# Optimization experiments

Measured on AMD Instinct MI355X. Metric: run time of the kernel, lower is better.

The kernel has to match this reference:

```python
import jax, jax.numpy as jnp
import numpy as np

B = 8192
MAX_ATOMS = 768
EPS = 1e-7


def setup_inputs() -> dict:
    key = jax.random.key(0)
    k1, k2, k3 = jax.random.split(key, 3)
    inp = jax.random.normal(k1, (B, 3 * MAX_ATOMS), dtype=jnp.float32)
    tgt = jax.random.normal(k2, (B, 3 * MAX_ATOMS), dtype=jnp.float32)
    # variable atom counts; keep >= MAX_ATOMS//2 so centering/division is well-posed
    num_atoms = jax.random.randint(k3, (B,), MAX_ATOMS // 2, MAX_ATOMS + 1, dtype=jnp.int64)
    return {"input": inp, "target": tgt, "num_atoms": num_atoms}


def _kabsch_rmsd(inp, tgt, num_atoms):
    b = inp.shape[0]
    m = inp.shape[1] // 3
    X = inp.reshape(b, m, 3)
    Y = tgt.reshape(b, m, 3)
    mask = (jnp.arange(m)[None, :] < num_atoms[:, None])[..., None]  # [B, M, 1]
    n = num_atoms.astype(inp.dtype)[:, None]  # [B, 1]
    # center over the valid atoms of each sample
    Xc = (X - (jnp.where(mask, X, 0).sum(axis=1) / n)[:, None, :])
    Yc = (Y - (jnp.where(mask, Y, 0).sum(axis=1) / n)[:, None, :])
    Xc = jnp.where(mask, Xc, 0)
    Yc = jnp.where(mask, Yc, 0)
    # 3x3 correlation matrix per sample (Kabsch)
    R = jnp.einsum('bai,baj->bij', Xc, Yc)  # [B, 3, 3]
    s = jnp.linalg.svd(R, compute_uv=False)  # [B, 3], descending
    d = jnp.sign(jnp.linalg.det(R))  # proper-rotation correction
    trace = s[:, 0] + s[:, 1] + d * s[:, 2]
    e = jnp.sum(Xc * Xc, axis=(1, 2)) + jnp.sum(Yc * Yc, axis=(1, 2)) - 2.0 * trace
    n1 = num_atoms.astype(inp.dtype)
    return jnp.sqrt(jnp.maximum(e, 0.0) / n1 + EPS)


def reference(input, target, num_atoms):
    return _kabsch_rmsd(input, target, num_atoms)
```

## Files before the change

kernel.cpp:

```cpp
#include <hip/hip_runtime.h>
#include <math.h>

#ifndef M_PI
#define M_PI 3.14159265358979323846
#endif

#define MA 768

__device__ __forceinline__ float wred64(float v) {
#pragma unroll
    for (int off = 32; off; off >>= 1) v += __shfl_xor(v, off, 64);
    return v;
}

__global__ __launch_bounds__(256) void kabsch_rmsd_kernel(
    const float* __restrict__ inp, const float* __restrict__ tgt,
    const int* __restrict__ natoms, float* __restrict__ out)
{
    const int wave = threadIdx.x >> 6;
    const int lane = threadIdx.x & 63;
    const int b = blockIdx.x * 4 + wave;
    const int n = natoms[b];
    const float* __restrict__ X = inp + (size_t)b * (3 * MA);
    const float* __restrict__ Y = tgt + (size_t)b * (3 * MA);

    float sx0 = 0.f, sx1 = 0.f, sx2 = 0.f;
    float sy0 = 0.f, sy1 = 0.f, sy2 = 0.f;
    float c00 = 0.f, c01 = 0.f, c02 = 0.f;
    float c10 = 0.f, c11 = 0.f, c12 = 0.f;
    float c20 = 0.f, c21 = 0.f, c22 = 0.f;
    float nx2 = 0.f, ny2 = 0.f;

    auto acc = [&](float x0, float x1, float x2, float y0, float y1, float y2) {
        sx0 += x0; sx1 += x1; sx2 += x2;
        sy0 += y0; sy1 += y1; sy2 += y2;
        c00 = fmaf(x0, y0, c00); c01 = fmaf(x0, y1, c01); c02 = fmaf(x0, y2, c02);
        c10 = fmaf(x1, y0, c10); c11 = fmaf(x1, y1, c11); c12 = fmaf(x1, y2, c12);
        c20 = fmaf(x2, y0, c20); c21 = fmaf(x2, y1, c21); c22 = fmaf(x2, y2, c22);
        nx2 = fmaf(x0, x0, nx2); nx2 = fmaf(x1, x1, nx2); nx2 = fmaf(x2, x2, nx2);
        ny2 = fmaf(y0, y0, ny2); ny2 = fmaf(y1, y1, ny2); ny2 = fmaf(y2, y2, ny2);
    };

#pragma unroll
    for (int it = 0; it < 3; ++it) {
        const int base = it * 256 + lane * 4;
        if (base < n) {
            const float4* px = (const float4*)(X + 3 * base);
            const float4* py = (const float4*)(Y + 3 * base);
            float4 fx0 = px[0], fx1 = px[1], fx2 = px[2];
            float4 fy0 = py[0], fy1 = py[1], fy2 = py[2];

            acc(fx0.x, fx0.y, fx0.z, fy0.x, fy0.y, fy0.z);
            {
                bool v = (base + 1) < n;
                float x0 = v ? fx0.w : 0.f, x1 = v ? fx1.x : 0.f, x2 = v ? fx1.y : 0.f;
                float y0 = v ? fy0.w : 0.f, y1 = v ? fy1.x : 0.f, y2 = v ? fy1.y : 0.f;
                acc(x0, x1, x2, y0, y1, y2);
            }
            {
                bool v = (base + 2) < n;
                float x0 = v ? fx1.z : 0.f, x1 = v ? fx1.w : 0.f, x2 = v ? fx2.x : 0.f;
                float y0 = v ? fy1.z : 0.f, y1 = v ? fy1.w : 0.f, y2 = v ? fy2.x : 0.f;
                acc(x0, x1, x2, y0, y1, y2);
            }
            {
                bool v = (base + 3) < n;
                float x0 = v ? fx2.y : 0.f, x1 = v ? fx2.z : 0.f, x2 = v ? fx2.w : 0.f;
                float y0 = v ? fy2.y : 0.f, y1 = v ? fy2.z : 0.f, y2 = v ? fy2.w : 0.f;
                acc(x0, x1, x2, y0, y1, y2);
            }
        }
    }

    sx0 = wred64(sx0); sx1 = wred64(sx1); sx2 = wred64(sx2);
    sy0 = wred64(sy0); sy1 = wred64(sy1); sy2 = wred64(sy2);
    c00 = wred64(c00); c01 = wred64(c01); c02 = wred64(c02);
    c10 = wred64(c10); c11 = wred64(c11); c12 = wred64(c12);
    c20 = wred64(c20); c21 = wred64(c21); c22 = wred64(c22);
    nx2 = wred64(nx2); ny2 = wred64(ny2);

    if (lane == 0) {
        const double dn = (double)n;

        double R00 = (double)c00 - (double)sx0 * (double)sy0 / dn;
        double R01 = (double)c01 - (double)sx0 * (double)sy1 / dn;
        double R02 = (double)c02 - (double)sx0 * (double)sy2 / dn;
        double R10 = (double)c10 - (double)sx1 * (double)sy0 / dn;
        double R11 = (double)c11 - (double)sx1 * (double)sy1 / dn;
        double R12 = (double)c12 - (double)sx1 * (double)sy2 / dn;
        double R20 = (double)c20 - (double)sx2 * (double)sy0 / dn;
        double R21 = (double)c21 - (double)sx2 * (double)sy1 / dn;
        double R22 = (double)c22 - (double)sx2 * (double)sy2 / dn;
        double ex = (double)nx2 -
            ((double)sx0 * sx0 + (double)sx1 * sx1 + (double)sx2 * sx2) / dn;
        double ey = (double)ny2 -
            ((double)sy0 * sy0 + (double)sy1 * sy1 + (double)sy2 * sy2) / dn;

        double A00 = R00 * R00 + R10 * R10 + R20 * R20;
        double A11 = R01 * R01 + R11 * R11 + R21 * R21;
        double A22 = R02 * R02 + R12 * R12 + R22 * R22;
        double A01 = R00 * R01 + R10 * R11 + R20 * R21;
        double A02 = R00 * R02 + R10 * R12 + R20 * R22;
        double A12 = R01 * R02 + R11 * R12 + R21 * R22;

        double detR = R00 * (R11 * R22 - R12 * R21)
                    - R01 * (R10 * R22 - R12 * R20)
                    + R02 * (R10 * R21 - R11 * R20);

        double q = (A00 + A11 + A22) / 3.0;
        double p1 = A01 * A01 + A02 * A02 + A12 * A12;
        double b00 = A00 - q, b11 = A11 - q, b22 = A22 - q;
        double p2 = b00 * b00 + b11 * b11 + b22 * b22 + 2.0 * p1;
        double e0, e1, e2;
        if (p2 <= 0.0) {
            e0 = e1 = e2 = q;
        } else {
            double p = sqrt(p2 / 6.0);
            double ip = 1.0 / p;
            double B00 = b00 * ip, B11 = b11 * ip, B22 = b22 * ip;
            double B01 = A01 * ip, B02 = A02 * ip, B12 = A12 * ip;
            double detB = B00 * (B11 * B22 - B12 * B12)
                        - B01 * (B01 * B22 - B12 * B02)
                        + B02 * (B01 * B12 - B11 * B02);
            double r = 0.5 * detB;
            r = fmin(1.0, fmax(-1.0, r));
            double phi = acos(r) / 3.0;
            e0 = q + 2.0 * p * cos(phi);
            e2 = q + 2.0 * p * cos(phi + 2.0 * M_PI / 3.0);
            e1 = 3.0 * q - e0 - e2;
        }
        double s0 = sqrt(fmax(e0, 0.0));
        double s1 = sqrt(fmax(e1, 0.0));
        double s2 = sqrt(fmax(e2, 0.0));
        double d = (detR > 0.0) ? 1.0 : ((detR < 0.0) ? -1.0 : 0.0);
        double tr = s0 + s1 + d * s2;
        double e = ex + ey - 2.0 * tr;
        out[b] = (float)sqrt(fmax(e, 0.0) / dn + 1e-7);
    }
}

extern "C" void kernel_launch(void* const* d_in, const int* in_sizes, int n_in,
                              void* d_out, int out_size, void* d_ws, size_t ws_size,
                              hipStream_t stream) {
    const float* inp = (const float*)d_in[0];
    const float* tgt = (const float*)d_in[1];
    const int* natoms = (const int*)d_in[2];
    float* out = (float*)d_out;
    (void)d_ws; (void)ws_size; (void)n_in; (void)in_sizes;
    kabsch_rmsd_kernel<<<dim3(out_size / 4), dim3(256), 0, stream>>>(inp, tgt, natoms, out);
}
```

Before: 29.72 us.

## Split Kabsch into reduction and per-thread eigen finish kernels with DPP reductions

The single kernel is split in two. The first reduces per-sample sums using DPP row operations instead of shuffle-xor and writes 17 partial sums per sample to workspace in SoA layout. The second kernel runs the double-precision 3x3 eigen and SVD finish with one thread per sample, so the serial lane-0 tail no longer stalls each wave. In exchange it adds a second launch and a workspace round-trip, and it hardcodes NB=8192.

```diff
diff --git a/kernel.cpp b/kernel.cpp
--- a/kernel.cpp
+++ b/kernel.cpp
@@ -6,16 +6,21 @@
 #endif
 
 #define MA 768
+#define NB 8192
 
-__device__ __forceinline__ float wred64(float v) {
-#pragma unroll
-    for (int off = 32; off; off >>= 1) v += __shfl_xor(v, off, 64);
+__device__ __forceinline__ float dpp_red_add(float v) {
+    v += __int_as_float(__builtin_amdgcn_update_dpp(0, __float_as_int(v), 0x111, 0xf, 0xf, true));
+    v += __int_as_float(__builtin_amdgcn_update_dpp(0, __float_as_int(v), 0x112, 0xf, 0xf, true));
+    v += __int_as_float(__builtin_amdgcn_update_dpp(0, __float_as_int(v), 0x114, 0xf, 0xe, true));
+    v += __int_as_float(__builtin_amdgcn_update_dpp(0, __float_as_int(v), 0x118, 0xf, 0xc, true));
+    v += __int_as_float(__builtin_amdgcn_update_dpp(0, __float_as_int(v), 0x142, 0xa, 0xf, true));
+    v += __int_as_float(__builtin_amdgcn_update_dpp(0, __float_as_int(v), 0x143, 0xc, 0xf, true));
     return v;
 }
 
-__global__ __launch_bounds__(256) void kabsch_rmsd_kernel(
+__global__ __launch_bounds__(256) void kabsch_reduce_kernel(
     const float* __restrict__ inp, const float* __restrict__ tgt,
-    const int* __restrict__ natoms, float* __restrict__ out)
+    const int* __restrict__ natoms, float* __restrict__ ws)
 {
     const int wave = threadIdx.x >> 6;
     const int lane = threadIdx.x & 63;
@@ -53,90 +58,108 @@
             acc(fx0.x, fx0.y, fx0.z, fy0.x, fy0.y, fy0.z);
             {
                 bool v = (base + 1) < n;
-                float x0 = v ? fx0.w : 0.f, x1 = v ? fx1.x : 0.f, x2 = v ? fx1.y : 0.f;
-                float y0 = v ? fy0.w : 0.f, y1 = v ? fy1.x : 0.f, y2 = v ? fy1.y : 0.f;
-                acc(x0, x1, x2, y0, y1, y2);
+                acc(v ? fx0.w : 0.f, v ? fx1.x : 0.f, v ? fx1.y : 0.f,
+                    v ? fy0.w : 0.f, v ? fy1.x : 0.f, v ? fy1.y : 0.f);
             }
             {
                 bool v = (base + 2) < n;
-                float x0 = v ? fx1.z : 0.f, x1 = v ? fx1.w : 0.f, x2 = v ? fx2.x : 0.f;
-                float y0 = v ? fy1.z : 0.f, y1 = v ? fy1.w : 0.f, y2 = v ? fy2.x : 0.f;
-                acc(x0, x1, x2, y0, y1, y2);
+                acc(v ? fx1.z : 0.f, v ? fx1.w : 0.f, v ? fx2.x : 0.f,
+                    v ? fy1.z : 0.f, v ? fy1.w : 0.f, v ? fy2.x : 0.f);
             }
             {
                 bool v = (base + 3) < n;
-                float x0 = v ? fx2.y : 0.f, x1 = v ? fx2.z : 0.f, x2 = v ? fx2.w : 0.f;
-                float y0 = v ? fy2.y : 0.f, y1 = v ? fy2.z : 0.f, y2 = v ? fy2.w : 0.f;
-                acc(x0, x1, x2, y0, y1, y2);
+                acc(v ? fx2.y : 0.f, v ? fx2.z : 0.f, v ? fx2.w : 0.f,
+                    v ? fy2.y : 0.f, v ? fy2.z : 0.f, v ? fy2.w : 0.f);
             }
         }
     }
 
-    sx0 = wred64(sx0); sx1 = wred64(sx1); sx2 = wred64(sx2);
-    sy0 = wred64(sy0); sy1 = wred64(sy1); sy2 = wred64(sy2);
-    c00 = wred64(c00); c01 = wred64(c01); c02 = wred64(c02);
-    c10 = wred64(c10); c11 = wred64(c11); c12 = wred64(c12);
-    c20 = wred64(c20); c21 = wred64(c21); c22 = wred64(c22);
-    nx2 = wred64(nx2); ny2 = wred64(ny2);
+    sx0 = dpp_red_add(sx0); sx1 = dpp_red_add(sx1); sx2 = dpp_red_add(sx2);
+    sy0 = dpp_red_add(sy0); sy1 = dpp_red_add(sy1); sy2 = dpp_red_add(sy2);
+    c00 = dpp_red_add(c00); c01 = dpp_red_add(c01); c02 = dpp_red_add(c02);
+    c10 = dpp_red_add(c10); c11 = dpp_red_add(c11); c12 = dpp_red_add(c12);
+    c20 = dpp_red_add(c20); c21 = dpp_red_add(c21); c22 = dpp_red_add(c22);
+    nx2 = dpp_red_add(nx2); ny2 = dpp_red_add(ny2);
 
-    if (lane == 0) {
-        const double dn = (double)n;
+    if (lane == 63) {
+        ws[ 0 * NB + b] = sx0; ws[ 1 * NB + b] = sx1; ws[ 2 * NB + b] = sx2;
+        ws[ 3 * NB + b] = sy0; ws[ 4 * NB + b] = sy1; ws[ 5 * NB + b] = sy2;
+        ws[ 6 * NB + b] = c00; ws[ 7 * NB + b] = c01; ws[ 8 * NB + b] = c02;
+        ws[ 9 * NB + b] = c10; ws[10 * NB + b] = c11; ws[11 * NB + b] = c12;
+        ws[12 * NB + b] = c20; ws[13 * NB + b] = c21; ws[14 * NB + b] = c22;
+        ws[15 * NB + b] = nx2; ws[16 * NB + b] = ny2;
+    }
+}
 
-        double R00 = (double)c00 - (double)sx0 * (double)sy0 / dn;
-        double R01 = (double)c01 - (double)sx0 * (double)sy1 / dn;
-        double R02 = (double)c02 - (double)sx0 * (double)sy2 / dn;
-        double R10 = (double)c10 - (double)sx1 * (double)sy0 / dn;
-        double R11 = (double)c11 - (double)sx1 * (double)sy1 / dn;
-        double R12 = (double)c12 - (double)sx1 * (double)sy2 / dn;
-        double R20 = (double)c20 - (double)sx2 * (double)sy0 / dn;
-        double R21 = (double)c21 - (double)sx2 * (double)sy1 / dn;
-        double R22 = (double)c22 - (double)sx2 * (double)sy2 / dn;
-        double ex = (double)nx2 -
-            ((double)sx0 * sx0 + (double)sx1 * sx1 + (double)sx2 * sx2) / dn;
-        double ey = (double)ny2 -
-            ((double)sy0 * sy0 + (double)sy1 * sy1 + (double)sy2 * sy2) / dn;
+__global__ __launch_bounds__(256) void kabsch_finish_kernel(
+    const float* __restrict__ ws, const int* __restrict__ natoms,
+    float* __restrict__ out)
+{
+    const int b = blockIdx.x * 256 + threadIdx.x;
+    const int n = natoms[b];
+    const double dn = (double)n;
 
-        double A00 = R00 * R00 + R10 * R10 + R20 * R20;
-        double A11 = R01 * R01 + R11 * R11 + R21 * R21;
-        double A22 = R02 * R02 + R12 * R12 + R22 * R22;
-        double A01 = R00 * R01 + R10 * R11 + R20 * R21;
-        double A02 = R00 * R02 + R10 * R12 + R20 * R22;
-        double A12 = R01 * R02 + R11 * R12 + R21 * R22;
+    const float sx0 = ws[ 0 * NB + b], sx1 = ws[ 1 * NB + b], sx2 = ws[ 2 * NB + b];
+    const float sy0 = ws[ 3 * NB + b], sy1 = ws[ 4 * NB + b], sy2 = ws[ 5 * NB + b];
+    const float c00 = ws[ 6 * NB + b], c01 = ws[ 7 * NB + b], c02 = ws[ 8 * NB + b];
+    const float c10 = ws[ 9 * NB + b], c11 = ws[10 * NB + b], c12 = ws[11 * NB + b];
+    const float c20 = ws[12 * NB + b], c21 = ws[13 * NB + b], c22 = ws[14 * NB + b];
+    const float nx2 = ws[15 * NB + b], ny2 = ws[16 * NB + b];
 
-        double detR = R00 * (R11 * R22 - R12 * R21)
-                    - R01 * (R10 * R22 - R12 * R20)
-                    + R02 * (R10 * R21 - R11 * R20);
+    double R00 = (double)c00 - (double)sx0 * (double)sy0 / dn;
+    double R01 = (double)c01 - (double)sx0 * (double)sy1 / dn;
+    double R02 = (double)c02 - (double)sx0 * (double)sy2 / dn;
+    double R10 = (double)c10 - (double)sx1 * (double)sy0 / dn;
+    double R11 = (double)c11 - (double)sx1 * (double)sy1 / dn;
+    double R12 = (double)c12 - (double)sx1 * (double)sy2 / dn;
+    double R20 = (double)c20 - (double)sx2 * (double)sy0 / dn;
+    double R21 = (double)c21 - (double)sx2 * (double)sy1 / dn;
+    double R22 = (double)c22 - (double)sx2 * (double)sy2 / dn;
+    double ex = (double)nx2 -
+        ((double)sx0 * sx0 + (double)sx1 * sx1 + (double)sx2 * sx2) / dn;
+    double ey = (double)ny2 -
+        ((double)sy0 * sy0 + (double)sy1 * sy1 + (double)sy2 * sy2) / dn;
 
-        double q = (A00 + A11 + A22) / 3.0;
-        double p1 = A01 * A01 + A02 * A02 + A12 * A12;
-        double b00 = A00 - q, b11 = A11 - q, b22 = A22 - q;
-        double p2 = b00 * b00 + b11 * b11 + b22 * b22 + 2.0 * p1;
-        double e0, e1, e2;
-        if (p2 <= 0.0) {
-            e0 = e1 = e2 = q;
-        } else {
-            double p = sqrt(p2 / 6.0);
-            double ip = 1.0 / p;
-            double B00 = b00 * ip, B11 = b11 * ip, B22 = b22 * ip;
-            double B01 = A01 * ip, B02 = A02 * ip, B12 = A12 * ip;
-            double detB = B00 * (B11 * B22 - B12 * B12)
-                        - B01 * (B01 * B22 - B12 * B02)
-                        + B02 * (B01 * B12 - B11 * B02);
-            double r = 0.5 * detB;
-            r = fmin(1.0, fmax(-1.0, r));
-            double phi = acos(r) / 3.0;
-            e0 = q + 2.0 * p * cos(phi);
-            e2 = q + 2.0 * p * cos(phi + 2.0 * M_PI / 3.0);
-            e1 = 3.0 * q - e0 - e2;
-        }
-        double s0 = sqrt(fmax(e0, 0.0));
-        double s1 = sqrt(fmax(e1, 0.0));
-        double s2 = sqrt(fmax(e2, 0.0));
-        double d = (detR > 0.0) ? 1.0 : ((detR < 0.0) ? -1.0 : 0.0);
-        double tr = s0 + s1 + d * s2;
-        double e = ex + ey - 2.0 * tr;
-        out[b] = (float)sqrt(fmax(e, 0.0) / dn + 1e-7);
+    double A00 = R00 * R00 + R10 * R10 + R20 * R20;
+    double A11 = R01 * R01 + R11 * R11 + R21 * R21;
+    double A22 = R02 * R02 + R12 * R12 + R22 * R22;
+    double A01 = R00 * R01 + R10 * R11 + R20 * R21;
+    double A02 = R00 * R02 + R10 * R12 + R20 * R22;
+    double A12 = R01 * R02 + R11 * R12 + R21 * R22;
+
+    double detR = R00 * (R11 * R22 - R12 * R21)
+                - R01 * (R10 * R22 - R12 * R20)
+                + R02 * (R10 * R21 - R11 * R20);
+
+    double q = (A00 + A11 + A22) / 3.0;
+    double p1 = A01 * A01 + A02 * A02 + A12 * A12;
+    double b00 = A00 - q, b11 = A11 - q, b22 = A22 - q;
+    double p2 = b00 * b00 + b11 * b11 + b22 * b22 + 2.0 * p1;
+    double e0, e1, e2;
+    if (p2 <= 0.0) {
+        e0 = e1 = e2 = q;
+    } else {
+        double p = sqrt(p2 / 6.0);
+        double ip = 1.0 / p;
+        double B00 = b00 * ip, B11 = b11 * ip, B22 = b22 * ip;
+        double B01 = A01 * ip, B02 = A02 * ip, B12 = A12 * ip;
+        double detB = B00 * (B11 * B22 - B12 * B12)
+                    - B01 * (B01 * B22 - B12 * B02)
+                    + B02 * (B01 * B12 - B11 * B02);
+        double r = 0.5 * detB;
+        r = fmin(1.0, fmax(-1.0, r));
+        double phi = acos(r) / 3.0;
+        e0 = q + 2.0 * p * cos(phi);
+        e2 = q + 2.0 * p * cos(phi + 2.0 * M_PI / 3.0);
+        e1 = 3.0 * q - e0 - e2;
     }
+    double s0 = sqrt(fmax(e0, 0.0));
+    double s1 = sqrt(fmax(e1, 0.0));
+    double s2 = sqrt(fmax(e2, 0.0));
+    double d = (detR > 0.0) ? 1.0 : ((detR < 0.0) ? -1.0 : 0.0);
+    double tr = s0 + s1 + d * s2;
+    double e = ex + ey - 2.0 * tr;
+    out[b] = (float)sqrt(fmax(e, 0.0) / dn + 1e-7);
 }
 
 extern "C" void kernel_launch(void* const* d_in, const int* in_sizes, int n_in,
@@ -146,6 +169,8 @@
     const float* tgt = (const float*)d_in[1];
     const int* natoms = (const int*)d_in[2];
     float* out = (float*)d_out;
-    (void)d_ws; (void)ws_size; (void)n_in; (void)in_sizes;
-    kabsch_rmsd_kernel<<<dim3(out_size / 4), dim3(256), 0, stream>>>(inp, tgt, natoms, out);
+    float* ws = (float*)d_ws;
+    (void)ws_size; (void)n_in; (void)in_sizes;
+    kabsch_reduce_kernel<<<dim3(out_size / 4), dim3(256), 0, stream>>>(inp, tgt, natoms, ws);
+    kabsch_finish_kernel<<<dim3(out_size / 256), dim3(256), 0, stream>>>(ws, natoms, out);
 }
```

New measurement: 28.09 us. -5.5%, faster.
